# Optimization experiments

Measured on AMD Instinct MI355X. Metric: run time of the kernel, lower is better.

## Reference

```python
import jax, jax.numpy as jnp
import numpy as np

B, S, D, H = 2, 2048, 1024, 16
DK = D // H

def setup_inputs() -> dict:
    key = jax.random.key(0)
    ks = jax.random.split(key, 9)
    def lin(k, fan_in):
        bound = 1.0 / np.sqrt(fan_in)
        kw, kb = jax.random.split(k)
        w = jax.random.uniform(kw, (D, D), jnp.float32, -bound, bound)
        b = jax.random.uniform(kb, (D,), jnp.float32, -bound, bound)
        return w, b
    Wq_w, Wq_b = lin(ks[0], D)
    Wk_w, Wk_b = lin(ks[1], D)
    Wv_w, Wv_b = lin(ks[2], D)
    Wo_w, Wo_b = lin(ks[3], D)
    x = jax.random.normal(ks[4], (B, S, D), jnp.float32)
    mask = jnp.ones((B, 1, 1, S), jnp.int32)
    return {"x": x, "mask": mask,
            "Wq_w": Wq_w, "Wq_b": Wq_b, "Wk_w": Wk_w, "Wk_b": Wk_b,
            "Wv_w": Wv_w, "Wv_b": Wv_b, "Wo_w": Wo_w, "Wo_b": Wo_b}

def reference(x, mask, Wq_w, Wq_b, Wk_w, Wk_b, Wv_w, Wv_b, Wo_w, Wo_b):
    b, s, d = x.shape
    def split_heads(t):  # [B,S,D] -> [B,H,S,DK]
        return t.reshape(b, s, H, DK).transpose(0, 2, 1, 3)
    Q = split_heads(x @ Wq_w.T + Wq_b)
    K = split_heads(x @ Wk_w.T + Wk_b)
    V = split_heads(x @ Wv_w.T + Wv_b)
    scale = 1.0 / jnp.sqrt(jnp.float32(DK))
    scores = jnp.einsum('bhqd,bhkd->bhqk', Q, K) * scale  # [B,H,S,S]
    scores = jnp.where(mask == 0, jnp.float32(-1e9), scores)
    attn = jax.nn.softmax(scores, axis=-1)
    context = jnp.einsum('bhqk,bhkd->bhqd', attn, V)  # [B,H,S,DK]
    context = context.transpose(0, 2, 1, 3).reshape(b, s, d)
    return context @ Wo_w.T + Wo_b
```

## Files before the change

### kernel.cpp

```cpp
#include <hip/hip_runtime.h>
#include <hip/hip_bf16.h>


#define DEV __device__ __forceinline__

typedef __bf16 bf16_t;
typedef __bf16 bf16x4 __attribute__((ext_vector_type(4)));
typedef __bf16 bf16x8 __attribute__((ext_vector_type(8)));
typedef float f32x4 __attribute__((ext_vector_type(4)));
typedef float f32x16 __attribute__((ext_vector_type(16)));
typedef unsigned int u32;

constexpr int Ss = 2048, Dd = 1024, Hh = 16, DKk = 64;

DEV void gload_lds16(const void* g, void* l) {
  __builtin_amdgcn_global_load_lds(
      (__attribute__((address_space(1))) void*)(g),
      (__attribute__((address_space(3))) void*)(l), 16, 0, 0);
}

DEV bf16_t f2b(float v) { return (bf16_t)v; }

DEV u32 cvtpk(float lo, float hi) {
  u32 r;
  asm("v_cvt_pk_bf16_f32 %0, %1, %2" : "=v"(r) : "v"(lo), "v"(hi));
  return r;
}

DEV void swap32(u32& a, u32& b) {
  asm("v_permlane32_swap_b32 %0, %1" : "+v"(a), "+v"(b));
}

DEV void cvt16_core(const float* src, bf16_t* dst) {
  const float4* s4 = (const float4*)src;
  float4 a = s4[0], b = s4[1], c = s4[2], d = s4[3];
  bf16x8 lo = {f2b(a.x), f2b(a.y), f2b(a.z), f2b(a.w), f2b(b.x), f2b(b.y), f2b(b.z), f2b(b.w)};
  bf16x8 hi = {f2b(c.x), f2b(c.y), f2b(c.z), f2b(c.w), f2b(d.x), f2b(d.y), f2b(d.z), f2b(d.w)};
  *(bf16x8*)dst = lo;
  *(bf16x8*)(dst + 8) = hi;
}

__global__ __launch_bounds__(256) void cvt16(const float* __restrict__ x,
                                             bf16_t* __restrict__ xb) {
  size_t i = ((size_t)blockIdx.x * 256 + threadIdx.x) * 16;
  cvt16_core(x + i, xb + i);
}

__global__ __launch_bounds__(256) void cvt_all(
    const float* __restrict__ x,
    const float* __restrict__ wq, const float* __restrict__ wk,
    const float* __restrict__ wv, const float* __restrict__ wo,
    bf16_t* __restrict__ xb, bf16_t* __restrict__ Wb) {
  size_t i = ((size_t)blockIdx.x * 256 + threadIdx.x) * 16;
  const size_t XN = (size_t)4 << 20;
  if (i < XN) {
    cvt16_core(x + i, xb + i);
  } else {
    size_t j = i - XN;
    int z = (int)(j >> 20);
    size_t o = j & (((size_t)1 << 20) - 1);
    const float* s = (z == 0) ? wq : ((z == 1) ? wk : ((z == 2) ? wv : wo));
    cvt16_core(s + o, Wb + j);
  }
}

template <bool WB16>
__global__ __launch_bounds__(256) void gemm_qkv(
    const bf16_t* __restrict__ A,
    const float* __restrict__ W0, const float* __restrict__ W1, const float* __restrict__ W2,
    const bf16_t* __restrict__ Wb,
    const float* __restrict__ b0, const float* __restrict__ b1, const float* __restrict__ b2,
    bf16_t* __restrict__ o0, bf16_t* __restrict__ o1, bf16_t* __restrict__ o2) {
  const int z = blockIdx.z;
  const float* Wf = (z == 0) ? W0 : ((z == 1) ? W1 : W2);
  const bf16_t* Wbf = Wb + (size_t)z * (1u << 20);
  const float* bias = (z == 0) ? b0 : ((z == 1) ? b1 : b2);
  bf16_t* out = (z == 0) ? o0 : ((z == 1) ? o1 : o2);
  const float scl = (z == 0) ? 0.125f : 1.0f;

  __shared__ __align__(16) bf16_t As[128 * 32];
  __shared__ __align__(16) bf16_t Ws[128 * 32];

  const int tid = threadIdx.x;
  const int lane = tid & 63, w = tid >> 6;
  const int quad = lane >> 4, c = lane & 15;
  const int wm = w >> 1, wn = w & 1;
  const int m0 = blockIdx.y * 128, n0 = blockIdx.x * 128;
  const int trow = tid >> 1, tcol = (tid & 1) * 16;
  const int srow = lane >> 2, scol = (lane & 3) * 8;

  const f32x4 vzero = {0.f, 0.f, 0.f, 0.f};
  f32x4 acc[4][4];
  for (int i = 0; i < 4; i++)
    for (int j = 0; j < 4; j++) acc[i][j] = vzero;

  for (int k0 = 0; k0 < 1024; k0 += 32) {
    for (int r = 0; r < 2; r++) {
      int row = r * 64 + w * 16;
      gload_lds16(&A[(size_t)(m0 + row + srow) * 1024 + k0 + scol], &As[row * 32]);
      if (WB16)
        gload_lds16(&Wbf[(size_t)(n0 + row + srow) * 1024 + k0 + scol], &Ws[row * 32]);
    }
    if (!WB16)
      cvt16_core(&Wf[(size_t)(n0 + trow) * 1024 + k0 + tcol], &Ws[trow * 32 + tcol]);
    __syncthreads();

    bf16x8 af[4], bfr[4];
    for (int i = 0; i < 4; i++)
      af[i] = *(const bf16x8*)&As[(wm * 64 + i * 16 + c) * 32 + quad * 8];
    for (int j = 0; j < 4; j++)
      bfr[j] = *(const bf16x8*)&Ws[(wn * 64 + j * 16 + c) * 32 + quad * 8];
    for (int i = 0; i < 4; i++)
      for (int j = 0; j < 4; j++)
        acc[i][j] = __builtin_amdgcn_mfma_f32_16x16x32_bf16(af[i], bfr[j], acc[i][j], 0, 0, 0);
    __syncthreads();
  }

  for (int j = 0; j < 4; j++) {
    int n = n0 + wn * 64 + j * 16 + c;
    float bv = bias[n];
    for (int i = 0; i < 4; i++) {
      int mbase = m0 + wm * 64 + i * 16 + quad * 4;
      int b_ = mbase >> 11, s_ = mbase & 2047;
      int h_ = n >> 6, dk_ = n & 63;
      if (z < 2) {
        for (int r = 0; r < 4; r++)
          out[((size_t)(b_ * Hh + h_) * Ss + (s_ + r)) * DKk + dk_] =
              f2b((acc[i][j][r] + bv) * scl);
      } else {
        bf16x4 pk;
        for (int r = 0; r < 4; r++) pk[r] = f2b(acc[i][j][r] + bv);
        *(bf16x4*)&out[((size_t)(b_ * Hh + h_) * DKk + dk_) * Ss + s_] = pk;
      }
    }
  }
}

__global__ __launch_bounds__(256) void attn_fwd(
    const bf16_t* __restrict__ Q, const bf16_t* __restrict__ K,
    const bf16_t* __restrict__ Vt, const int* __restrict__ mask,
    bf16_t* __restrict__ ctx) {
  __shared__ __align__(16) bf16_t Ks[2][64 * 64];
  __shared__ __align__(16) bf16_t Vts[2][64 * 64];

  const int tid = threadIdx.x, lane = tid & 63, w = tid >> 6;
  const int m = lane & 31, hi = lane >> 5;

  const int fid = (int)(blockIdx.y * gridDim.x + blockIdx.x);
  const int xcd = fid & 7, j_ = fid >> 3;
  const int bh = xcd * 4 + (j_ >> 4);
  const int qblk = j_ & 15;

  const int b_ = bh >> 4, h_ = bh & 15;
  const int q0 = qblk * 128 + w * 32;
  const size_t head = (size_t)bh * Ss * DKk;
  const int* maskb = mask + b_ * Ss;

  const int sr = lane >> 3;
  const int gc = (lane & 7) ^ sr;

  for (int r = 0; r < 2; r++) {
    int row = r * 32 + w * 8;
    gload_lds16(&K[head + (size_t)(row + sr) * 64 + gc * 8], &Ks[0][row * 64]);
    gload_lds16(&Vt[head + (size_t)(row + sr) * Ss + gc * 8], &Vts[0][row * 64]);
  }

  bf16x8 qf[4];
#pragma unroll
  for (int ks = 0; ks < 4; ks++)
    qf[ks] = *(const bf16x8*)&Q[head + (size_t)(q0 + m) * 64 + ks * 16 + hi * 8];

  const bf16_t oneb = f2b(1.0f);
  const bf16x8 ones = {oneb, oneb, oneb, oneb, oneb, oneb, oneb, oneb};

  f32x16 o0, o1, ol;
#pragma unroll
  for (int i = 0; i < 16; i++) { o0[i] = 0.f; o1[i] = 0.f; ol[i] = 0.f; }

  constexpr int NT = Ss / 64;
  for (int kt = 0; kt < NT; kt++) {
    const int cur = kt & 1;
    __syncthreads();

    int mv = maskb[kt * 64 + lane];

    if (kt + 1 < NT) {
      int nxt = cur ^ 1;
      for (int r = 0; r < 2; r++) {
        int row = r * 32 + w * 8;
        gload_lds16(&K[head + (size_t)((kt + 1) * 64 + row + sr) * 64 + gc * 8],
                    &Ks[nxt][row * 64]);
        gload_lds16(&Vt[head + (size_t)(row + sr) * Ss + (kt + 1) * 64 + gc * 8],
                    &Vts[nxt][row * 64]);
      }
    }

    f32x16 sc[2];
#pragma unroll
    for (int i = 0; i < 16; i++) { sc[0][i] = 0.f; sc[1][i] = 0.f; }

    __builtin_amdgcn_s_setprio(1);
#pragma unroll
    for (int ks = 0; ks < 4; ks++) {
      const int pc = ((ks * 2 + hi) ^ (m & 7)) * 8;
      bf16x8 k0 = *(const bf16x8*)&Ks[cur][m * 64 + pc];
      bf16x8 k1 = *(const bf16x8*)&Ks[cur][(32 + m) * 64 + pc];
      sc[0] = __builtin_amdgcn_mfma_f32_32x32x16_bf16(k0, qf[ks], sc[0], 0, 0, 0);
      sc[1] = __builtin_amdgcn_mfma_f32_32x32x16_bf16(k1, qf[ks], sc[1], 0, 0, 0);
    }
    __builtin_amdgcn_s_setprio(0);

    unsigned long long bits = __ballot(mv != 0);
    if (bits == ~0ull) {
#pragma unroll
      for (int nt = 0; nt < 2; nt++)
#pragma unroll
        for (int i = 0; i < 16; i++) sc[nt][i] = __expf(sc[nt][i]);
    } else {
#pragma unroll
      for (int nt = 0; nt < 2; nt++) {
        u32 wb = (u32)(bits >> (nt * 32));
        u32 wsh = hi ? (wb >> 4) : wb;
#pragma unroll
        for (int i = 0; i < 16; i++) {
          int bitpos = 8 * (i >> 2) + (i & 3);
          sc[nt][i] = ((wsh >> bitpos) & 1u) ? __expf(sc[nt][i]) : 0.f;
        }
      }
    }

    __builtin_amdgcn_s_setprio(1);
#pragma unroll
    for (int t = 0; t < 4; t++) {
      const int nt = t >> 1, gA = 2 * (t & 1), gB = gA + 1;
      u32 a0 = cvtpk(sc[nt][4 * gA + 0], sc[nt][4 * gA + 1]);
      u32 a1 = cvtpk(sc[nt][4 * gA + 2], sc[nt][4 * gA + 3]);
      u32 b0 = cvtpk(sc[nt][4 * gB + 0], sc[nt][4 * gB + 1]);
      u32 b1 = cvtpk(sc[nt][4 * gB + 2], sc[nt][4 * gB + 3]);
      swap32(a0, b0);
      swap32(a1, b1);
      int4 wv = {(int)a0, (int)a1, (int)b0, (int)b1};
      bf16x8 pa = __builtin_bit_cast(bf16x8, wv);

      ol = __builtin_amdgcn_mfma_f32_32x32x16_bf16(pa, ones, ol, 0, 0, 0);
      const int pc = ((t * 2 + hi) ^ (m & 7)) * 8;
      bf16x8 v0 = *(const bf16x8*)&Vts[cur][m * 64 + pc];
      bf16x8 v1 = *(const bf16x8*)&Vts[cur][(32 + m) * 64 + pc];
      o0 = __builtin_amdgcn_mfma_f32_32x32x16_bf16(pa, v0, o0, 0, 0, 0);
      o1 = __builtin_amdgcn_mfma_f32_32x32x16_bf16(pa, v1, o1, 0, 0, 0);
    }
    __builtin_amdgcn_s_setprio(0);
  }

  f32x16 inv;
#pragma unroll
  for (int r = 0; r < 16; r++) inv[r] = 1.0f / ol[r];
#pragma unroll
  for (int r = 0; r < 16; r++) {
    int s_ = q0 + (r & 3) + 8 * (r >> 2) + 4 * hi;
    size_t base = ((size_t)(b_ * Ss + s_)) * Dd + h_ * 64;
    ctx[base + m] = f2b(o0[r] * inv[r]);
    ctx[base + 32 + m] = f2b(o1[r] * inv[r]);
  }
}

template <bool WB16>
__global__ __launch_bounds__(256) void gemm_out(
    const bf16_t* __restrict__ A, const float* __restrict__ Wf,
    const bf16_t* __restrict__ Wb, const float* __restrict__ bias,
    float* __restrict__ out) {
  __shared__ __align__(16) bf16_t As[64 * 32];
  __shared__ __align__(16) bf16_t Ws[128 * 32];

  const int tid = threadIdx.x;
  const int lane = tid & 63, w = tid >> 6;
  const int quad = lane >> 4, c = lane & 15;
  const int wm = w >> 1, wn = w & 1;
  const int m0 = blockIdx.y * 64, n0 = blockIdx.x * 128;
  const int trow = tid >> 1, tcol = (tid & 1) * 16;
  const int srow = lane >> 2, scol = (lane & 3) * 8;

  const f32x4 vzero = {0.f, 0.f, 0.f, 0.f};
  f32x4 acc[2][4];
  for (int i = 0; i < 2; i++)
    for (int j = 0; j < 4; j++) acc[i][j] = vzero;

  for (int k0 = 0; k0 < 1024; k0 += 32) {
    gload_lds16(&A[(size_t)(m0 + w * 16 + srow) * 1024 + k0 + scol], &As[(w * 16) * 32]);
    if (WB16) {
      for (int r = 0; r < 2; r++) {
        int row = r * 64 + w * 16;
        gload_lds16(&Wb[(size_t)(n0 + row + srow) * 1024 + k0 + scol], &Ws[row * 32]);
      }
    } else {
      cvt16_core(&Wf[(size_t)(n0 + trow) * 1024 + k0 + tcol], &Ws[trow * 32 + tcol]);
    }
    __syncthreads();

    bf16x8 af[2], bfr[4];
    for (int i = 0; i < 2; i++)
      af[i] = *(const bf16x8*)&As[(wm * 32 + i * 16 + c) * 32 + quad * 8];
    for (int j = 0; j < 4; j++)
      bfr[j] = *(const bf16x8*)&Ws[(wn * 64 + j * 16 + c) * 32 + quad * 8];
    for (int i = 0; i < 2; i++)
      for (int j = 0; j < 4; j++)
        acc[i][j] = __builtin_amdgcn_mfma_f32_16x16x32_bf16(af[i], bfr[j], acc[i][j], 0, 0, 0);
    __syncthreads();
  }

  for (int j = 0; j < 4; j++) {
    int n = n0 + wn * 64 + j * 16 + c;
    float bv = bias[n];
    for (int i = 0; i < 2; i++) {
      int mbase = m0 + wm * 32 + i * 16 + quad * 4;
      for (int r = 0; r < 4; r++)
        out[(size_t)(mbase + r) * 1024 + n] = acc[i][j][r] + bv;
    }
  }
}

extern "C" void kernel_launch(void* const* d_in, const int* in_sizes, int n_in,
                              void* d_out, int out_size, void* d_ws, size_t ws_size,
                              hipStream_t stream) {
  const float* x  = (const float*)d_in[0];
  const int* mask = (const int*)d_in[1];
  const float* Wq = (const float*)d_in[2];
  const float* bq = (const float*)d_in[3];
  const float* Wk = (const float*)d_in[4];
  const float* bk = (const float*)d_in[5];
  const float* Wv = (const float*)d_in[6];
  const float* bv = (const float*)d_in[7];
  const float* Wo = (const float*)d_in[8];
  const float* bo = (const float*)d_in[9];
  float* out = (float*)d_out;

  bf16_t* ws = (bf16_t*)d_ws;
  const size_t QKV_ELEMS = (size_t)2 * Hh * Ss * DKk;
  bf16_t* xb  = ws;
  bf16_t* Qb  = ws + QKV_ELEMS;
  bf16_t* Kb  = ws + 2 * QKV_ELEMS;
  bf16_t* Vt  = ws + 3 * QKV_ELEMS;
  bf16_t* Wb  = ws + 4 * QKV_ELEMS;
  bf16_t* ctx = xb;

  const bool wb16 = ws_size >= (size_t)40 * 1024 * 1024;

  if (wb16) {
    cvt_all<<<dim3(2048), 256, 0, stream>>>(x, Wq, Wk, Wv, Wo, xb, Wb);
    gemm_qkv<true><<<dim3(8, 32, 3), 256, 0, stream>>>(
        xb, Wq, Wk, Wv, Wb, bq, bk, bv, Qb, Kb, Vt);
  } else {
    cvt16<<<dim3(1024), 256, 0, stream>>>(x, xb);
    gemm_qkv<false><<<dim3(8, 32, 3), 256, 0, stream>>>(
        xb, Wq, Wk, Wv, ws , bq, bk, bv, Qb, Kb, Vt);
  }
  attn_fwd<<<dim3(Ss / 128, 2 * Hh), 256, 0, stream>>>(Qb, Kb, Vt, mask, ctx);
  if (wb16)
    gemm_out<true><<<dim3(8, 64), 256, 0, stream>>>(ctx, Wo, Wb + 3 * (1u << 20), bo, out);
  else
    gemm_out<false><<<dim3(8, 64), 256, 0, stream>>>(ctx, Wo, ws , bo, out);
}
```

Baseline: 199.7 us.

## Split attention KV range across two wave groups, swizzle GEMM blocks, use exp2

The attention kernel now runs 512 threads per block: two groups of four waves each handle half the key sequence with their own double-buffered LDS tiles, and the partial outputs and row sums are combined through shared memory at the end. The Q scale folds in log2(e) so the raw v_exp_f32 (exp2) instruction can replace __expf. The QKV and output GEMMs remap block indices in an XCD-aware order to improve L2 locality. The split doubles wave-level parallelism per query tile and shortens each wave's serial loop, at the cost of more LDS, an extra reduction step and higher register pressure under the new launch bounds.

```diff
diff --git a/kernel.cpp b/kernel.cpp
--- a/kernel.cpp
+++ b/kernel.cpp
@@ -29,6 +29,12 @@
 
 DEV void swap32(u32& a, u32& b) {
   asm("v_permlane32_swap_b32 %0, %1" : "+v"(a), "+v"(b));
+}
+
+DEV float exp2_fast(float x) {
+  float r;
+  asm("v_exp_f32 %0, %1" : "=v"(r) : "v"(x));
+  return r;
 }
 
 DEV void cvt16_core(const float* src, bf16_t* dst) {
@@ -71,12 +77,15 @@
     const bf16_t* __restrict__ Wb,
     const float* __restrict__ b0, const float* __restrict__ b1, const float* __restrict__ b2,
     bf16_t* __restrict__ o0, bf16_t* __restrict__ o1, bf16_t* __restrict__ o2) {
-  const int z = blockIdx.z;
+  const int fid = (int)((blockIdx.z * gridDim.y + blockIdx.y) * gridDim.x + blockIdx.x);
+  const int swz = (fid & 7) * 96 + (fid >> 3);
+  const int bx = swz & 7, by = (swz >> 3) & 31, z = swz >> 8;
+
   const float* Wf = (z == 0) ? W0 : ((z == 1) ? W1 : W2);
   const bf16_t* Wbf = Wb + (size_t)z * (1u << 20);
   const float* bias = (z == 0) ? b0 : ((z == 1) ? b1 : b2);
   bf16_t* out = (z == 0) ? o0 : ((z == 1) ? o1 : o2);
-  const float scl = (z == 0) ? 0.125f : 1.0f;
+  const float scl = (z == 0) ? 0.18033688f : 1.0f;
 
   __shared__ __align__(16) bf16_t As[128 * 32];
   __shared__ __align__(16) bf16_t Ws[128 * 32];
@@ -85,7 +94,7 @@
   const int lane = tid & 63, w = tid >> 6;
   const int quad = lane >> 4, c = lane & 15;
   const int wm = w >> 1, wn = w & 1;
-  const int m0 = blockIdx.y * 128, n0 = blockIdx.x * 128;
+  const int m0 = by * 128, n0 = bx * 128;
   const int trow = tid >> 1, tcol = (tid & 1) * 16;
   const int srow = lane >> 2, scol = (lane & 3) * 8;
 
@@ -136,14 +145,14 @@
   }
 }
 
-__global__ __launch_bounds__(256) void attn_fwd(
+__global__ __launch_bounds__(512, 4) void attn_fwd(
     const bf16_t* __restrict__ Q, const bf16_t* __restrict__ K,
     const bf16_t* __restrict__ Vt, const int* __restrict__ mask,
     bf16_t* __restrict__ ctx) {
-  __shared__ __align__(16) bf16_t Ks[2][64 * 64];
-  __shared__ __align__(16) bf16_t Vts[2][64 * 64];
+  __shared__ __align__(16) bf16_t smem[2][2][2][64 * 64];
 
   const int tid = threadIdx.x, lane = tid & 63, w = tid >> 6;
+  const int g = w >> 2, wl = w & 3;
   const int m = lane & 31, hi = lane >> 5;
 
   const int fid = (int)(blockIdx.y * gridDim.x + blockIdx.x);
@@ -152,17 +161,21 @@
   const int qblk = j_ & 15;
 
   const int b_ = bh >> 4, h_ = bh & 15;
-  const int q0 = qblk * 128 + w * 32;
+  const int q0 = qblk * 128 + wl * 32;
   const size_t head = (size_t)bh * Ss * DKk;
-  const int* maskb = mask + b_ * Ss;
+  const int* maskb = mask + b_ * Ss + g * 1024;
+  const int kbase = g * 16;
+
+  bf16_t (*Ksg)[64 * 64] = smem[0][g];
+  bf16_t (*Vtg)[64 * 64] = smem[1][g];
 
   const int sr = lane >> 3;
   const int gc = (lane & 7) ^ sr;
 
   for (int r = 0; r < 2; r++) {
-    int row = r * 32 + w * 8;
-    gload_lds16(&K[head + (size_t)(row + sr) * 64 + gc * 8], &Ks[0][row * 64]);
-    gload_lds16(&Vt[head + (size_t)(row + sr) * Ss + gc * 8], &Vts[0][row * 64]);
+    int row = r * 32 + wl * 8;
+    gload_lds16(&K[head + (size_t)(kbase * 64 + row + sr) * 64 + gc * 8], &Ksg[0][row * 64]);
+    gload_lds16(&Vt[head + (size_t)(row + sr) * Ss + kbase * 64 + gc * 8], &Vtg[0][row * 64]);
   }
 
   bf16x8 qf[4];
@@ -177,21 +190,22 @@
 #pragma unroll
   for (int i = 0; i < 16; i++) { o0[i] = 0.f; o1[i] = 0.f; ol[i] = 0.f; }
 
-  constexpr int NT = Ss / 64;
-  for (int kt = 0; kt < NT; kt++) {
-    const int cur = kt & 1;
+  constexpr int NTg = 16;
+  for (int it = 0; it < NTg; it++) {
+    const int cur = it & 1;
     __syncthreads();
 
-    int mv = maskb[kt * 64 + lane];
-
-    if (kt + 1 < NT) {
+    int mv = maskb[it * 64 + lane];
+
+    if (it + 1 < NTg) {
       int nxt = cur ^ 1;
+      int t = kbase + it + 1;
       for (int r = 0; r < 2; r++) {
-        int row = r * 32 + w * 8;
-        gload_lds16(&K[head + (size_t)((kt + 1) * 64 + row + sr) * 64 + gc * 8],
-                    &Ks[nxt][row * 64]);
-        gload_lds16(&Vt[head + (size_t)(row + sr) * Ss + (kt + 1) * 64 + gc * 8],
-                    &Vts[nxt][row * 64]);
+        int row = r * 32 + wl * 8;
+        gload_lds16(&K[head + (size_t)(t * 64 + row + sr) * 64 + gc * 8],
+                    &Ksg[nxt][row * 64]);
+        gload_lds16(&Vt[head + (size_t)(row + sr) * Ss + t * 64 + gc * 8],
+                    &Vtg[nxt][row * 64]);
       }
     }
 
@@ -203,8 +217,8 @@
 #pragma unroll
     for (int ks = 0; ks < 4; ks++) {
       const int pc = ((ks * 2 + hi) ^ (m & 7)) * 8;
-      bf16x8 k0 = *(const bf16x8*)&Ks[cur][m * 64 + pc];
-      bf16x8 k1 = *(const bf16x8*)&Ks[cur][(32 + m) * 64 + pc];
+      bf16x8 k0 = *(const bf16x8*)&Ksg[cur][m * 64 + pc];
+      bf16x8 k1 = *(const bf16x8*)&Ksg[cur][(32 + m) * 64 + pc];
       sc[0] = __builtin_amdgcn_mfma_f32_32x32x16_bf16(k0, qf[ks], sc[0], 0, 0, 0);
       sc[1] = __builtin_amdgcn_mfma_f32_32x32x16_bf16(k1, qf[ks], sc[1], 0, 0, 0);
     }
@@ -215,7 +229,7 @@
 #pragma unroll
       for (int nt = 0; nt < 2; nt++)
 #pragma unroll
-        for (int i = 0; i < 16; i++) sc[nt][i] = __expf(sc[nt][i]);
+        for (int i = 0; i < 16; i++) sc[nt][i] = exp2_fast(sc[nt][i]);
     } else {
 #pragma unroll
       for (int nt = 0; nt < 2; nt++) {
@@ -224,7 +238,7 @@
 #pragma unroll
         for (int i = 0; i < 16; i++) {
           int bitpos = 8 * (i >> 2) + (i & 3);
-          sc[nt][i] = ((wsh >> bitpos) & 1u) ? __expf(sc[nt][i]) : 0.f;
+          sc[nt][i] = ((wsh >> bitpos) & 1u) ? exp2_fast(sc[nt][i]) : 0.f;
         }
       }
     }
@@ -244,23 +258,51 @@
 
       ol = __builtin_amdgcn_mfma_f32_32x32x16_bf16(pa, ones, ol, 0, 0, 0);
       const int pc = ((t * 2 + hi) ^ (m & 7)) * 8;
-      bf16x8 v0 = *(const bf16x8*)&Vts[cur][m * 64 + pc];
-      bf16x8 v1 = *(const bf16x8*)&Vts[cur][(32 + m) * 64 + pc];
+      bf16x8 v0 = *(const bf16x8*)&Vtg[cur][m * 64 + pc];
+      bf16x8 v1 = *(const bf16x8*)&Vtg[cur][(32 + m) * 64 + pc];
       o0 = __builtin_amdgcn_mfma_f32_32x32x16_bf16(pa, v0, o0, 0, 0, 0);
       o1 = __builtin_amdgcn_mfma_f32_32x32x16_bf16(pa, v1, o1, 0, 0, 0);
     }
     __builtin_amdgcn_s_setprio(0);
   }
 
-  f32x16 inv;
-#pragma unroll
-  for (int r = 0; r < 16; r++) inv[r] = 1.0f / ol[r];
-#pragma unroll
-  for (int r = 0; r < 16; r++) {
-    int s_ = q0 + (r & 3) + 8 * (r >> 2) + 4 * hi;
-    size_t base = ((size_t)(b_ * Ss + s_)) * Dd + h_ * 64;
-    ctx[base + m] = f2b(o0[r] * inv[r]);
-    ctx[base + 32 + m] = f2b(o1[r] * inv[r]);
+  __syncthreads();
+  f32x4* cmb = (f32x4*)smem;
+  if (g == 1) {
+#pragma unroll
+    for (int c = 0; c < 4; c++) {
+      f32x4 t0 = {o0[4 * c], o0[4 * c + 1], o0[4 * c + 2], o0[4 * c + 3]};
+      f32x4 t1 = {o1[4 * c], o1[4 * c + 1], o1[4 * c + 2], o1[4 * c + 3]};
+      f32x4 t2 = {ol[4 * c], ol[4 * c + 1], ol[4 * c + 2], ol[4 * c + 3]};
+      cmb[(c + 0) * 256 + wl * 64 + lane] = t0;
+      cmb[(c + 4) * 256 + wl * 64 + lane] = t1;
+      cmb[(c + 8) * 256 + wl * 64 + lane] = t2;
+    }
+  }
+  __syncthreads();
+  if (g == 0) {
+#pragma unroll
+    for (int c = 0; c < 4; c++) {
+      f32x4 p0 = cmb[(c + 0) * 256 + wl * 64 + lane];
+      f32x4 p1 = cmb[(c + 4) * 256 + wl * 64 + lane];
+      f32x4 p2 = cmb[(c + 8) * 256 + wl * 64 + lane];
+#pragma unroll
+      for (int k = 0; k < 4; k++) {
+        o0[4 * c + k] += p0[k];
+        o1[4 * c + k] += p1[k];
+        ol[4 * c + k] += p2[k];
+      }
+    }
+    f32x16 inv;
+#pragma unroll
+    for (int r = 0; r < 16; r++) inv[r] = 1.0f / ol[r];
+#pragma unroll
+    for (int r = 0; r < 16; r++) {
+      int s_ = q0 + (r & 3) + 8 * (r >> 2) + 4 * hi;
+      size_t base = ((size_t)(b_ * Ss + s_)) * Dd + h_ * 64;
+      ctx[base + m] = f2b(o0[r] * inv[r]);
+      ctx[base + 32 + m] = f2b(o1[r] * inv[r]);
+    }
   }
 }
 
@@ -272,11 +314,15 @@
   __shared__ __align__(16) bf16_t As[64 * 32];
   __shared__ __align__(16) bf16_t Ws[128 * 32];
 
+  const int fid = (int)(blockIdx.y * gridDim.x + blockIdx.x);
+  const int swz = (fid & 7) * 64 + (fid >> 3);
+  const int bx = swz & 7, by = swz >> 3;
+
   const int tid = threadIdx.x;
   const int lane = tid & 63, w = tid >> 6;
   const int quad = lane >> 4, c = lane & 15;
   const int wm = w >> 1, wn = w & 1;
-  const int m0 = blockIdx.y * 64, n0 = blockIdx.x * 128;
+  const int m0 = by * 64, n0 = bx * 128;
   const int trow = tid >> 1, tcol = (tid & 1) * 16;
   const int srow = lane >> 2, scol = (lane & 3) * 8;
 
@@ -354,7 +400,7 @@
     gemm_qkv<false><<<dim3(8, 32, 3), 256, 0, stream>>>(
         xb, Wq, Wk, Wv, ws , bq, bk, bv, Qb, Kb, Vt);
   }
-  attn_fwd<<<dim3(Ss / 128, 2 * Hh), 256, 0, stream>>>(Qb, Kb, Vt, mask, ctx);
+  attn_fwd<<<dim3(Ss / 128, 2 * Hh), 512, 0, stream>>>(Qb, Kb, Vt, mask, ctx);
   if (wb16)
     gemm_out<true><<<dim3(8, 64), 256, 0, stream>>>(ctx, Wo, Wb + 3 * (1u << 20), bo, out);
   else
```

After: 217.3 us. 1.09x slower.
